# Performance work log

Hardware: AMD Instinct MI355X
Metric: run time of the kernel (lower is better)

Reference implementation:

```python
import jax, jax.numpy as jnp
import numpy as np

N_NODES = 100000
N_EDGES = 400000
IN_FEATS = 64
H_FEATS = 128
INTER = 128
NUM_CLASSES = 64


def setup_inputs() -> dict:
    key = jax.random.key(0)
    ks = jax.random.split(key, 32)
    inp = {}
    inp['gate_type'] = jax.random.randint(ks[0], (N_NODES,), 0, IN_FEATS)
    inp['src'] = jax.random.randint(ks[1], (N_EDGES,), 0, N_NODES)
    inp['dst'] = jax.random.randint(ks[2], (N_EDGES,), 0, N_NODES)
    inp['src_idx'] = jax.random.uniform(ks[3], (N_EDGES,), dtype=jnp.float32)
    inp['dst_idx'] = jax.random.uniform(ks[4], (N_EDGES,), dtype=jnp.float32)
    inp['rev'] = jax.random.uniform(ks[5], (N_EDGES,), dtype=jnp.float32)
    inp['emb'] = jax.random.normal(ks[6], (IN_FEATS, IN_FEATS), dtype=jnp.float32) * 0.05
    dims = [(IN_FEATS, H_FEATS), (H_FEATS, H_FEATS), (H_FEATS, H_FEATS), (H_FEATS, H_FEATS), (H_FEATS, NUM_CLASSES)]
    k = 7
    for i, (fi, fo) in enumerate(dims, 1):
        # xavier-normal-like scaling
        inp[f'w1_{i}'] = jax.random.normal(ks[k], (INTER, fi + 3), dtype=jnp.float32) * np.float32(np.sqrt(2.0 / (fi + 3 + INTER))); k += 1
        inp[f'w2_{i}'] = jax.random.normal(ks[k], (fo, fi + INTER), dtype=jnp.float32) * np.float32(np.sqrt(2.0 / (fi + INTER + fo))); k += 1
        inp[f'b2_{i}'] = jnp.zeros((fo,), dtype=jnp.float32); k += 1
    return inp


def _qconv(h, src, dst, w_edge, W1, W2, b2):
    # message: concat src node feats with edge feats -> [E, d+3]
    m = jnp.concatenate([h[src], w_edge], axis=1)
    # linear1 (no bias) + leaky_relu (torch default slope 0.01)
    tmp = jax.nn.leaky_relu(m @ W1.T, negative_slope=0.01)  # [E, inter]
    # mean-reduce per destination node (isolated nodes -> zeros, matching DGL)
    s = jax.ops.segment_sum(tmp, dst, num_segments=h.shape[0])
    cnt = jax.ops.segment_sum(jnp.ones((dst.shape[0],), tmp.dtype), dst, num_segments=h.shape[0])
    h_N = s / jnp.maximum(cnt, 1.0)[:, None]
    # linear2 on [h, h_N]
    return jnp.concatenate([h, h_N], axis=1) @ W2.T + b2


def reference(gate_type, src, dst, src_idx, dst_idx, rev, emb,
              w1_1, w2_1, b2_1, w1_2, w2_2, b2_2, w1_3, w2_3, b2_3,
              w1_4, w2_4, b2_4, w1_5, w2_5, b2_5):
    h = emb[gate_type]  # [N, in_feats]
    w_edge = jnp.stack([src_idx, dst_idx, rev], axis=1)  # [E, 3]
    layers = [(w1_1, w2_1, b2_1), (w1_2, w2_2, b2_2), (w1_3, w2_3, b2_3),
              (w1_4, w2_4, b2_4), (w1_5, w2_5, b2_5)]
    for i, (W1, W2, b2) in enumerate(layers):
        h = _qconv(h, src, dst, w_edge, W1, W2, b2)
        if i < 4:
            h = jax.nn.relu(h)
    return h
```

## Files before the change

kernel.cpp:

```cpp
#include <hip/hip_runtime.h>
#include <hip/hip_fp16.h>

typedef __attribute__((ext_vector_type(8))) short short8;
typedef __attribute__((ext_vector_type(4))) float f32x4;
typedef unsigned short u16;

__device__ __forceinline__ u16 f2bf(float f) {
    unsigned u = __float_as_uint(f);
    unsigned r = ((u >> 16) & 1) + 0x7FFFu;
    return (u16)((u + r) >> 16);
}

__device__ __forceinline__ void gload_lds16(const void* g, void* l) {
    __builtin_amdgcn_global_load_lds((const __attribute__((address_space(1))) unsigned int*)g,
                                     (__attribute__((address_space(3))) unsigned int*)l,
                                     16, 0, 0);
}

__device__ __forceinline__ unsigned pk_fma(unsigned a, unsigned b, unsigned c) {
    unsigned d;
    asm("v_pk_fma_f16 %0, %1, %2, %3" : "=v"(d) : "v"(a), "v"(b), "v"(c));
    return d;
}
__device__ __forceinline__ unsigned pk_mul(unsigned a, unsigned b) {
    unsigned d;
    asm("v_pk_mul_f16 %0, %1, %2" : "=v"(d) : "v"(a), "v"(b));
    return d;
}
__device__ __forceinline__ unsigned pk_max(unsigned a, unsigned b) {
    unsigned d;
    asm("v_pk_max_f16 %0, %1, %2" : "=v"(d) : "v"(a), "v"(b));
    return d;
}


__global__ void k_count(const int* __restrict__ dst, int* __restrict__ cnt, int E) {
    int i = blockIdx.x * 256 + threadIdx.x;
    if (i < E) atomicAdd(&cnt[dst[i]], 1);
}

__global__ void k_scan1(const int* __restrict__ cnt, int* __restrict__ partial, int N) {
    __shared__ int sm[256];
    int idx = blockIdx.x * 256 + threadIdx.x;
    sm[threadIdx.x] = (idx < N) ? cnt[idx] : 0;
    __syncthreads();
    for (int s = 128; s > 0; s >>= 1) {
        if (threadIdx.x < s) sm[threadIdx.x] += sm[threadIdx.x + s];
        __syncthreads();
    }
    if (threadIdx.x == 0) partial[blockIdx.x] = sm[0];
}

__global__ void k_scan2(int* __restrict__ partial, int nb) {
    __shared__ int sm[512];
    int t = threadIdx.x;
    sm[t] = (t < nb) ? partial[t] : 0;
    __syncthreads();
    for (int off = 1; off < 512; off <<= 1) {
        int v = (t >= off) ? sm[t - off] : 0;
        __syncthreads();
        sm[t] += v;
        __syncthreads();
    }
    if (t < nb) partial[t] = (t == 0) ? 0 : sm[t - 1];
}

__global__ void k_scan3(const int* __restrict__ cnt, const int* __restrict__ partial,
                        int* __restrict__ row_off, int* __restrict__ cursor,
                        float* __restrict__ invdeg, int N, int E) {
    __shared__ int sm[256];
    int idx = blockIdx.x * 256 + threadIdx.x;
    int v = (idx < N) ? cnt[idx] : 0;
    sm[threadIdx.x] = v;
    __syncthreads();
    for (int off = 1; off < 256; off <<= 1) {
        int u = (threadIdx.x >= off) ? sm[threadIdx.x - off] : 0;
        __syncthreads();
        sm[threadIdx.x] += u;
        __syncthreads();
    }
    if (idx < N) {
        int excl = partial[blockIdx.x] + sm[threadIdx.x] - v;
        row_off[idx] = excl;
        cursor[idx] = excl;
        invdeg[idx] = 1.0f / (float)((v > 1) ? v : 1);
    }
    if (idx == 0) row_off[N] = E;
}

__global__ void k_scatter(const int* __restrict__ dst, const int* __restrict__ src,
                          const float* __restrict__ sidx, const float* __restrict__ didx,
                          const float* __restrict__ rev,
                          int* __restrict__ cursor, int4* __restrict__ payload, int E) {
    int i = blockIdx.x * 256 + threadIdx.x;
    if (i < E) {
        int p = atomicAdd(&cursor[dst[i]], 1);
        unsigned hs = (unsigned)__half_as_ushort(__float2half_rn(sidx[i]));
        unsigned hd = (unsigned)__half_as_ushort(__float2half_rn(didx[i]));
        unsigned hr = (unsigned)__half_as_ushort(__float2half_rn(rev[i]));
        int4 v;
        v.x = src[i];
        v.y = (int)(hs * 0x10001u);
        v.z = (int)(hd * 0x10001u);
        v.w = (int)(hr * 0x10001u);
        payload[p] = v;
    }
}


__global__ void k_emb(const int* __restrict__ gt, const float* __restrict__ emb,
                      u16* __restrict__ h0, int N) {
    int i = blockIdx.x * 256 + threadIdx.x;
    if (i < N * 64) {
        int n = i >> 6, f = i & 63;
        h0[i] = f2bf(emb[(gt[n] << 6) | f]);
    }
}


struct WDesc {
    const float* src[10];
    u16* dst[10];
    int scols[10];
    int dcols[10];
    int n[10];
};

__global__ void k_wconv(WDesc d) {
    int seg = blockIdx.y;
    int idx = blockIdx.x * 256 + threadIdx.x;
    if (idx < d.n[seg]) {
        int dc = d.dcols[seg];
        int r = idx / dc, c = idx % dc;
        d.dst[seg][idx] = f2bf(d.src[seg][r * d.scols[seg] + c]);
    }
}

struct EDesc {
    const float* src[5];
    unsigned* dst[5];
    int ldw[5];
    int fi[5];
};

__global__ void k_wedge(EDesc d) {
    int l = blockIdx.x;
    int i = threadIdx.x;
    if (i < 192) {
        int c = i >> 6, j = i & 63;
        float a = d.src[l][(size_t)(2 * j) * d.ldw[l] + d.fi[l] + c];
        float b = d.src[l][(size_t)(2 * j + 1) * d.ldw[l] + d.fi[l] + c];
        unsigned lo = (unsigned)__half_as_ushort(__float2half_rn(a));
        unsigned hi = (unsigned)__half_as_ushort(__float2half_rn(b));
        d.dst[l][(c << 6) + j] = lo | (hi << 16);
    }
}


__global__ __launch_bounds__(256)
void k_edge(int N,
            const int* __restrict__ row_off, const int4* __restrict__ payload,
            const u16* __restrict__ g,
            const unsigned* __restrict__ W1h,
            const float* __restrict__ invdeg,
            u16* __restrict__ hN)
{
    const int t = threadIdx.x;
    const int lane = t & 63;
    const int fl = lane & 15;
    const int eg = lane >> 4;
    const int wid = blockIdx.x * (blockDim.x >> 6) + (t >> 6);
    const int nwtot = gridDim.x * (blockDim.x >> 6);
    const int per = (N + nwtot - 1) / nwtot;
    const int n0 = wid * per;
    if (n0 >= N) return;
    const int n1 = (n0 + per < N) ? (n0 + per) : N;

    const uint4 wa = *(const uint4*)&W1h[(fl << 2)];
    const uint4 wb = *(const uint4*)&W1h[64 + (fl << 2)];
    const uint4 wc = *(const uint4*)&W1h[128 + (fl << 2)];
    const unsigned c001 = ((unsigned)__half_as_ushort(__float2half_rn(0.01f))) * 0x10001u;

    int beg = row_off[n0];
    for (int n = n0; n < n1; ++n) {
        const int end = row_off[n + 1];
        float acc[8] = {0.f, 0.f, 0.f, 0.f, 0.f, 0.f, 0.f, 0.f};

        int p = beg + eg;
        int4 pl;
        if (p < end) pl = payload[p];
        while (p < end) {
            const int pn = p + 4;
            int4 plN = pl;
            if (pn < end) plN = payload[pn];
            const uint4 gv = *(const uint4*)(g + ((size_t)pl.x << 7) + (fl << 3));
            const unsigned si = (unsigned)pl.y;
            const unsigned di = (unsigned)pl.z;
            const unsigned rv = (unsigned)pl.w;
            unsigned v0 = pk_fma(wa.x, si, gv.x);
            unsigned v1 = pk_fma(wa.y, si, gv.y);
            unsigned v2 = pk_fma(wa.z, si, gv.z);
            unsigned v3 = pk_fma(wa.w, si, gv.w);
            v0 = pk_fma(wb.x, di, v0);
            v1 = pk_fma(wb.y, di, v1);
            v2 = pk_fma(wb.z, di, v2);
            v3 = pk_fma(wb.w, di, v3);
            v0 = pk_fma(wc.x, rv, v0);
            v1 = pk_fma(wc.y, rv, v1);
            v2 = pk_fma(wc.z, rv, v2);
            v3 = pk_fma(wc.w, rv, v3);
            v0 = pk_max(v0, pk_mul(v0, c001));
            v1 = pk_max(v1, pk_mul(v1, c001));
            v2 = pk_max(v2, pk_mul(v2, c001));
            v3 = pk_max(v3, pk_mul(v3, c001));
            const float2 f0 = __half22float2(*(const __half2*)&v0);
            const float2 f1 = __half22float2(*(const __half2*)&v1);
            const float2 f2 = __half22float2(*(const __half2*)&v2);
            const float2 f3 = __half22float2(*(const __half2*)&v3);
            acc[0] += f0.x; acc[1] += f0.y;
            acc[2] += f1.x; acc[3] += f1.y;
            acc[4] += f2.x; acc[5] += f2.y;
            acc[6] += f3.x; acc[7] += f3.y;
            p = pn;
            pl = plN;
        }

#pragma unroll
        for (int r = 0; r < 8; r++) {
            acc[r] += __shfl_xor(acc[r], 16, 64);
            acc[r] += __shfl_xor(acc[r], 32, 64);
        }

        if (eg == 0) {
            const float inv = invdeg[n];
            unsigned q0 = (unsigned)f2bf(acc[0] * inv) | ((unsigned)f2bf(acc[1] * inv) << 16);
            unsigned q1 = (unsigned)f2bf(acc[2] * inv) | ((unsigned)f2bf(acc[3] * inv) << 16);
            unsigned q2 = (unsigned)f2bf(acc[4] * inv) | ((unsigned)f2bf(acc[5] * inv) << 16);
            unsigned q3 = (unsigned)f2bf(acc[6] * inv) | ((unsigned)f2bf(acc[7] * inv) << 16);
            uint4 out = make_uint4(q0, q1, q2, q3);
            *(uint4*)(hN + ((size_t)n << 7) + (fl << 3)) = out;
        }
        beg = end;
    }
}


template<int K, int O, int SPLIT, int BIAS, int RELU, int OUTDT, int FUSE>
__global__ __launch_bounds__(512, 4)
void k_gemm(int M,
            const u16* __restrict__ A1, int lda1,
            const u16* __restrict__ A2, int lda2,
            const u16* __restrict__ W,
            const float* __restrict__ bias,
            void* __restrict__ Cout, int ldc,
            const u16* __restrict__ Wg,
            u16* __restrict__ Gout)
{
    constexpr int KP = K + 8;
    constexpr int HP = 136;
    constexpr int NF = O / 32;
    constexpr int WC = O / 2;
    __shared__ __align__(16) u16 Wlds[O * KP];
    __shared__ __align__(16) u16 Atile[128 * 32];

    const int t = threadIdx.x;
    const int m0 = blockIdx.x * 128;
    const int w = t >> 6, l = t & 63;
    const int wm = w & 3, wn = w >> 2;
    const int lr = l & 15, lh = l >> 4;

    for (int idx = t; idx < O * (K / 8); idx += 512) {
        int row = idx / (K / 8), ch = idx % (K / 8);
        uint4 v = *(const uint4*)(W + (size_t)row * K + ch * 8);
        *(uint4*)(&Wlds[row * KP + ch * 8]) = v;
    }

    f32x4 acc[2][NF];
#pragma unroll
    for (int mi = 0; mi < 2; mi++)
#pragma unroll
        for (int ni = 0; ni < NF; ni++) acc[mi][ni] = (f32x4){0.f, 0.f, 0.f, 0.f};

    __syncthreads();

    for (int kt = 0; kt < K / 32; ++kt) {
        const int k0 = kt * 32;
        const u16* Asrc;
        int lda, kof;
        if (k0 < SPLIT) { Asrc = A1; lda = lda1; kof = k0; }
        else            { Asrc = A2; lda = lda2; kof = k0 - SPLIT; }
        {
            int o = t * 16;
            int row = o >> 6;
            int m = m0 + row;
            m = (m < M) ? m : (M - 1);
            gload_lds16(Asrc + (size_t)m * lda + kof + ((t & 3) << 3), (void*)(Atile + (o >> 1)));
        }
        __syncthreads();

        short8 a[2], b[NF];
#pragma unroll
        for (int mi = 0; mi < 2; mi++)
            a[mi] = *(const short8*)(Atile + (wm * 32 + mi * 16 + lr) * 32 + lh * 8);
#pragma unroll
        for (int ni = 0; ni < NF; ni++)
            b[ni] = *(const short8*)(Wlds + (size_t)(wn * WC + ni * 16 + lr) * KP + k0 + lh * 8);
#pragma unroll
        for (int mi = 0; mi < 2; mi++)
#pragma unroll
            for (int ni = 0; ni < NF; ni++)
                acc[mi][ni] = __builtin_amdgcn_mfma_f32_16x16x32_bf16(a[mi], b[ni], acc[mi][ni], 0, 0, 0);
        __syncthreads();
    }

    if (FUSE) {
        for (int idx = t; idx < 128 * 16; idx += 512) {
            int row = idx >> 4, ch = idx & 15;
            uint4 v = *(const uint4*)(Wg + (size_t)row * 128 + ch * 8);
            *(uint4*)(&Wlds[row * HP + ch * 8]) = v;
        }
    }

    float bv[NF];
#pragma unroll
    for (int ni = 0; ni < NF; ni++)
        bv[ni] = BIAS ? bias[wn * WC + ni * 16 + lr] : 0.f;
#pragma unroll
    for (int mi = 0; mi < 2; mi++) {
#pragma unroll
        for (int i = 0; i < 4; i++) {
            int row = m0 + wm * 32 + mi * 16 + lh * 4 + i;
            if (row < M) {
#pragma unroll
                for (int ni = 0; ni < NF; ni++) {
                    float v = acc[mi][ni][i] + bv[ni];
                    if (RELU) v = fmaxf(v, 0.f);
                    int col = wn * WC + ni * 16 + lr;
                    if (FUSE || OUTDT == 1) ((u16*)Cout)[(size_t)row * ldc + col] = f2bf(v);
                    else if (OUTDT == 2)    ((__half*)Cout)[(size_t)row * ldc + col] = __float2half(v);
                    else                    ((float*)Cout)[(size_t)row * ldc + col] = v;
                }
            }
        }
    }

    if (FUSE) {
        __syncthreads();

        const u16* H = (const u16*)Cout;
        int hrow[2];
#pragma unroll
        for (int mi = 0; mi < 2; mi++) {
            int m = m0 + wm * 32 + mi * 16 + lr;
            hrow[mi] = (m < M) ? m : (M - 1);
        }

        f32x4 acc2[2][4];
#pragma unroll
        for (int mi = 0; mi < 2; mi++)
#pragma unroll
            for (int ni = 0; ni < 4; ni++) acc2[mi][ni] = (f32x4){0.f, 0.f, 0.f, 0.f};

#pragma unroll
        for (int kt = 0; kt < 4; ++kt) {
            const int k0 = kt * 32;
            short8 a[2], b[4];
#pragma unroll
            for (int mi = 0; mi < 2; mi++)
                a[mi] = *(const short8*)(H + (size_t)hrow[mi] * ldc + k0 + lh * 8);
#pragma unroll
            for (int ni = 0; ni < 4; ni++)
                b[ni] = *(const short8*)(Wlds + (size_t)(wn * 64 + ni * 16 + lr) * HP + k0 + lh * 8);
#pragma unroll
            for (int mi = 0; mi < 2; mi++)
#pragma unroll
                for (int ni = 0; ni < 4; ni++)
                    acc2[mi][ni] = __builtin_amdgcn_mfma_f32_16x16x32_bf16(a[mi], b[ni], acc2[mi][ni], 0, 0, 0);
        }

#pragma unroll
        for (int mi = 0; mi < 2; mi++) {
#pragma unroll
            for (int i = 0; i < 4; i++) {
                int row = m0 + wm * 32 + mi * 16 + lh * 4 + i;
                if (row < M) {
#pragma unroll
                    for (int ni = 0; ni < 4; ni++) {
                        int col = wn * 64 + ni * 16 + lr;
                        ((__half*)Gout)[(size_t)row * 128 + col] = __float2half(acc2[mi][ni][i]);
                    }
                }
            }
        }
    }
}


extern "C" void kernel_launch(void* const* d_in, const int* in_sizes, int n_in,
                              void* d_out, int out_size, void* d_ws, size_t ws_size,
                              hipStream_t stream)
{
    const int N = in_sizes[0];
    const int E = in_sizes[1];
    const int* gate = (const int*)d_in[0];
    const int* src = (const int*)d_in[1];
    const int* dst = (const int*)d_in[2];
    const float* sidx = (const float*)d_in[3];
    const float* didx = (const float*)d_in[4];
    const float* rev = (const float*)d_in[5];
    const float* emb = (const float*)d_in[6];
    const float* w1[5] = {(const float*)d_in[7], (const float*)d_in[10], (const float*)d_in[13],
                          (const float*)d_in[16], (const float*)d_in[19]};
    const float* w2[5] = {(const float*)d_in[8], (const float*)d_in[11], (const float*)d_in[14],
                          (const float*)d_in[17], (const float*)d_in[20]};
    const float* b2[5] = {(const float*)d_in[9], (const float*)d_in[12], (const float*)d_in[15],
                          (const float*)d_in[18], (const float*)d_in[21]};

    char* ws = (char*)d_ws;
    size_t off = 0;
    auto alloc = [&](size_t bytes) {
        void* p = ws + off;
        off = (off + bytes + 255) & ~(size_t)255;
        return p;
    };
    u16* hb0 = (u16*)alloc((size_t)N * 128 * 2);
    u16* hb1 = (u16*)alloc((size_t)N * 128 * 2);
    u16* hN = (u16*)alloc((size_t)N * 128 * 2);
    u16* g = (u16*)alloc((size_t)N * 128 * 2);
    int* cnt = (int*)alloc((size_t)N * 4);
    int* row_off = (int*)alloc((size_t)(N + 1) * 4);
    int* cursor = (int*)alloc((size_t)N * 4);
    int4* payload = (int4*)alloc((size_t)E * 16);
    int* partial = (int*)alloc(512 * 4);
    float* invd = (float*)alloc((size_t)N * 4);
    unsigned* w1h = (unsigned*)alloc(5 * 192 * 4);
    u16* w1b[5];
    u16* w2b[5];
    const int fis[5] = {64, 128, 128, 128, 128};
    for (int i = 0; i < 5; i++) w1b[i] = (u16*)alloc((size_t)128 * fis[i] * 2);
    for (int i = 0; i < 5; i++) {
        int fo = (i == 4) ? 64 : 128;
        w2b[i] = (u16*)alloc((size_t)fo * (fis[i] + 128) * 2);
    }

    WDesc wd;
    for (int i = 0; i < 5; i++) {
        wd.src[i] = w1[i]; wd.dst[i] = w1b[i];
        wd.scols[i] = fis[i] + 3; wd.dcols[i] = fis[i]; wd.n[i] = 128 * fis[i];
        int fo = (i == 4) ? 64 : 128;
        wd.src[5 + i] = w2[i]; wd.dst[5 + i] = w2b[i];
        wd.scols[5 + i] = fis[i] + 128; wd.dcols[5 + i] = fis[i] + 128;
        wd.n[5 + i] = fo * (fis[i] + 128);
    }
    k_wconv<<<dim3(128, 10), dim3(256), 0, stream>>>(wd);

    EDesc ed;
    for (int i = 0; i < 5; i++) {
        ed.src[i] = w1[i];
        ed.dst[i] = w1h + i * 192;
        ed.ldw[i] = fis[i] + 3;
        ed.fi[i] = fis[i];
    }
    k_wedge<<<dim3(5), dim3(192), 0, stream>>>(ed);

    hipMemsetAsync(cnt, 0, (size_t)N * 4, stream);
    k_count<<<dim3((E + 255) / 256), dim3(256), 0, stream>>>(dst, cnt, E);
    const int nb = (N + 255) / 256;
    k_scan1<<<dim3(nb), dim3(256), 0, stream>>>(cnt, partial, N);
    k_scan2<<<dim3(1), dim3(512), 0, stream>>>(partial, nb);
    k_scan3<<<dim3(nb), dim3(256), 0, stream>>>(cnt, partial, row_off, cursor, invd, N, E);
    k_scatter<<<dim3((E + 255) / 256), dim3(256), 0, stream>>>(dst, src, sidx, didx, rev, cursor, payload, E);
    k_emb<<<dim3((N * 64 + 255) / 256), dim3(256), 0, stream>>>(gate, emb, hb0, N);

    const int gg = (N + 127) / 128;
    const int eb = 2048;

    k_gemm<64, 128, 64, 0, 0, 2, 0><<<dim3(gg), dim3(512), 0, stream>>>(
        N, hb0, 64, (const u16*)nullptr, 0, w1b[0], (const float*)nullptr, g, 128,
        (const u16*)nullptr, (u16*)nullptr);
    k_edge<<<dim3(eb), dim3(256), 0, stream>>>(N, row_off, payload, g, w1h + 0 * 192, invd, hN);
    k_gemm<192, 128, 64, 1, 1, 1, 1><<<dim3(gg), dim3(512), 0, stream>>>(
        N, hb0, 64, hN, 128, w2b[0], b2[0], hb1, 128, w1b[1], g);

    u16* hcur = hb1;
    u16* hnxt = hb0;
    for (int l = 1; l < 4; ++l) {
        k_edge<<<dim3(eb), dim3(256), 0, stream>>>(N, row_off, payload, g, w1h + l * 192, invd, hN);
        k_gemm<256, 128, 128, 1, 1, 1, 1><<<dim3(gg), dim3(512), 0, stream>>>(
            N, hcur, 128, hN, 128, w2b[l], b2[l], hnxt, 128, w1b[l + 1], g);
        u16* tmp = hcur; hcur = hnxt; hnxt = tmp;
    }

    k_edge<<<dim3(eb), dim3(256), 0, stream>>>(N, row_off, payload, g, w1h + 4 * 192, invd, hN);
    k_gemm<256, 64, 128, 1, 0, 0, 0><<<dim3(gg), dim3(512), 0, stream>>>(
        N, hcur, 128, hN, 128, w2b[4], b2[4], (float*)d_out, 64,
        (const u16*)nullptr, (u16*)nullptr);
}
```

Before: 413.1 us.

## Interleave two destination nodes per wave and accumulate edge sums in packed fp16

```diff
diff --git a/kernel.cpp b/kernel.cpp
--- a/kernel.cpp
+++ b/kernel.cpp
@@ -30,6 +30,11 @@
 __device__ __forceinline__ unsigned pk_max(unsigned a, unsigned b) {
     unsigned d;
     asm("v_pk_max_f16 %0, %1, %2" : "=v"(d) : "v"(a), "v"(b));
+    return d;
+}
+__device__ __forceinline__ unsigned pk_add(unsigned a, unsigned b) {
+    unsigned d;
+    asm("v_pk_add_f16 %0, %1, %2" : "=v"(d) : "v"(a), "v"(b));
     return d;
 }
 
@@ -176,71 +181,123 @@
     if (n0 >= N) return;
     const int n1 = (n0 + per < N) ? (n0 + per) : N;
 
+    int roi = n0 + lane;
+    const int ro_l = row_off[(roi <= n1) ? roi : n1];
+
     const uint4 wa = *(const uint4*)&W1h[(fl << 2)];
     const uint4 wb = *(const uint4*)&W1h[64 + (fl << 2)];
     const uint4 wc = *(const uint4*)&W1h[128 + (fl << 2)];
     const unsigned c001 = ((unsigned)__half_as_ushort(__float2half_rn(0.01f))) * 0x10001u;
 
-    int beg = row_off[n0];
-    for (int n = n0; n < n1; ++n) {
-        const int end = row_off[n + 1];
-        float acc[8] = {0.f, 0.f, 0.f, 0.f, 0.f, 0.f, 0.f, 0.f};
-
-        int p = beg + eg;
-        int4 pl;
-        if (p < end) pl = payload[p];
-        while (p < end) {
-            const int pn = p + 4;
-            int4 plN = pl;
-            if (pn < end) plN = payload[pn];
-            const uint4 gv = *(const uint4*)(g + ((size_t)pl.x << 7) + (fl << 3));
-            const unsigned si = (unsigned)pl.y;
-            const unsigned di = (unsigned)pl.z;
-            const unsigned rv = (unsigned)pl.w;
-            unsigned v0 = pk_fma(wa.x, si, gv.x);
-            unsigned v1 = pk_fma(wa.y, si, gv.y);
-            unsigned v2 = pk_fma(wa.z, si, gv.z);
-            unsigned v3 = pk_fma(wa.w, si, gv.w);
-            v0 = pk_fma(wb.x, di, v0);
-            v1 = pk_fma(wb.y, di, v1);
-            v2 = pk_fma(wb.z, di, v2);
-            v3 = pk_fma(wb.w, di, v3);
-            v0 = pk_fma(wc.x, rv, v0);
-            v1 = pk_fma(wc.y, rv, v1);
-            v2 = pk_fma(wc.z, rv, v2);
-            v3 = pk_fma(wc.w, rv, v3);
-            v0 = pk_max(v0, pk_mul(v0, c001));
-            v1 = pk_max(v1, pk_mul(v1, c001));
-            v2 = pk_max(v2, pk_mul(v2, c001));
-            v3 = pk_max(v3, pk_mul(v3, c001));
-            const float2 f0 = __half22float2(*(const __half2*)&v0);
-            const float2 f1 = __half22float2(*(const __half2*)&v1);
-            const float2 f2 = __half22float2(*(const __half2*)&v2);
-            const float2 f3 = __half22float2(*(const __half2*)&v3);
-            acc[0] += f0.x; acc[1] += f0.y;
-            acc[2] += f1.x; acc[3] += f1.y;
-            acc[4] += f2.x; acc[5] += f2.y;
-            acc[6] += f3.x; acc[7] += f3.y;
-            p = pn;
-            pl = plN;
-        }
-
-#pragma unroll
-        for (int r = 0; r < 8; r++) {
-            acc[r] += __shfl_xor(acc[r], 16, 64);
-            acc[r] += __shfl_xor(acc[r], 32, 64);
-        }
-
+    int na, pa, ea, qa;
+    int4 pla;
+    uint4 gva;
+    unsigned accA[4] = {0u, 0u, 0u, 0u};
+    int nb_, pb, eb, qb;
+    int4 plb;
+    uint4 gvb;
+    unsigned accB[4] = {0u, 0u, 0u, 0u};
+
+    auto prime = [&](int n, int& p, int& e, int& q, int4& pl, uint4& gv) {
+        const int idx = n - n0;
+        const int b = __shfl(ro_l, idx, 64);
+        e = __shfl(ro_l, idx + 1, 64);
+        p = b + eg;
+        q = (e - b + 3) >> 2;
+        if (p < e) {
+            pl = payload[p];
+            gv = *(const uint4*)(g + ((size_t)pl.x << 7) + (fl << 3));
+        }
+    };
+
+    auto quadf = [&](const int4& pl, const uint4& gv, unsigned* acc) {
+        const unsigned si = (unsigned)pl.y;
+        const unsigned di = (unsigned)pl.z;
+        const unsigned rv = (unsigned)pl.w;
+        unsigned v0 = pk_fma(wa.x, si, gv.x);
+        unsigned v1 = pk_fma(wa.y, si, gv.y);
+        unsigned v2 = pk_fma(wa.z, si, gv.z);
+        unsigned v3 = pk_fma(wa.w, si, gv.w);
+        v0 = pk_fma(wb.x, di, v0);
+        v1 = pk_fma(wb.y, di, v1);
+        v2 = pk_fma(wb.z, di, v2);
+        v3 = pk_fma(wb.w, di, v3);
+        v0 = pk_fma(wc.x, rv, v0);
+        v1 = pk_fma(wc.y, rv, v1);
+        v2 = pk_fma(wc.z, rv, v2);
+        v3 = pk_fma(wc.w, rv, v3);
+        v0 = pk_max(v0, pk_mul(v0, c001));
+        v1 = pk_max(v1, pk_mul(v1, c001));
+        v2 = pk_max(v2, pk_mul(v2, c001));
+        v3 = pk_max(v3, pk_mul(v3, c001));
+        acc[0] = pk_add(acc[0], v0);
+        acc[1] = pk_add(acc[1], v1);
+        acc[2] = pk_add(acc[2], v2);
+        acc[3] = pk_add(acc[3], v3);
+    };
+
+    auto finishf = [&](int n, unsigned* acc) {
+#pragma unroll
+        for (int r = 0; r < 4; r++) {
+            acc[r] = pk_add(acc[r], (unsigned)__shfl_xor((int)acc[r], 16, 64));
+            acc[r] = pk_add(acc[r], (unsigned)__shfl_xor((int)acc[r], 32, 64));
+        }
         if (eg == 0) {
             const float inv = invdeg[n];
-            unsigned q0 = (unsigned)f2bf(acc[0] * inv) | ((unsigned)f2bf(acc[1] * inv) << 16);
-            unsigned q1 = (unsigned)f2bf(acc[2] * inv) | ((unsigned)f2bf(acc[3] * inv) << 16);
-            unsigned q2 = (unsigned)f2bf(acc[4] * inv) | ((unsigned)f2bf(acc[5] * inv) << 16);
-            unsigned q3 = (unsigned)f2bf(acc[6] * inv) | ((unsigned)f2bf(acc[7] * inv) << 16);
+            const float2 f0 = __half22float2(*(const __half2*)&acc[0]);
+            const float2 f1 = __half22float2(*(const __half2*)&acc[1]);
+            const float2 f2 = __half22float2(*(const __half2*)&acc[2]);
+            const float2 f3 = __half22float2(*(const __half2*)&acc[3]);
+            unsigned q0 = (unsigned)f2bf(f0.x * inv) | ((unsigned)f2bf(f0.y * inv) << 16);
+            unsigned q1 = (unsigned)f2bf(f1.x * inv) | ((unsigned)f2bf(f1.y * inv) << 16);
+            unsigned q2 = (unsigned)f2bf(f2.x * inv) | ((unsigned)f2bf(f2.y * inv) << 16);
+            unsigned q3 = (unsigned)f2bf(f3.x * inv) | ((unsigned)f2bf(f3.y * inv) << 16);
             uint4 out = make_uint4(q0, q1, q2, q3);
             *(uint4*)(hN + ((size_t)n << 7) + (fl << 3)) = out;
         }
-        beg = end;
+        acc[0] = acc[1] = acc[2] = acc[3] = 0u;
+    };
+
+    na = n0;
+    prime(na, pa, ea, qa, pla, gva);
+    nb_ = n0 + 1;
+    bool doneB = (nb_ >= n1);
+    if (!doneB) prime(nb_, pb, eb, qb, plb, gvb);
+    bool doneA = false;
+
+    while (!doneA || !doneB) {
+        if (!doneA) {
+            if (qa > 0) {
+                if (pa < ea) quadf(pla, gva, accA);
+                pa += 4;
+                qa--;
+                if (qa > 0 && pa < ea) {
+                    pla = payload[pa];
+                    gva = *(const uint4*)(g + ((size_t)pla.x << 7) + (fl << 3));
+                }
+            } else {
+                finishf(na, accA);
+                na += 2;
+                if (na < n1) prime(na, pa, ea, qa, pla, gva);
+                else doneA = true;
+            }
+        }
+        if (!doneB) {
+            if (qb > 0) {
+                if (pb < eb) quadf(plb, gvb, accB);
+                pb += 4;
+                qb--;
+                if (qb > 0 && pb < eb) {
+                    plb = payload[pb];
+                    gvb = *(const uint4*)(g + ((size_t)plb.x << 7) + (fl << 3));
+                }
+            } else {
+                finishf(nb_, accB);
+                nb_ += 2;
+                if (nb_ < n1) prime(nb_, pb, eb, qb, plb, gvb);
+                else doneB = true;
+            }
+        }
     }
 }
 
```

Result: slower. 451.3 us (+9.2%).

## Precompute per-gate-type layer-1 projection table and drop first GEMM

Applied to the files above, without the earlier changes.

```diff
diff --git a/kernel.cpp b/kernel.cpp
--- a/kernel.cpp
+++ b/kernel.cpp
@@ -108,12 +108,29 @@
 }
 
 
-__global__ void k_emb(const int* __restrict__ gt, const float* __restrict__ emb,
-                      u16* __restrict__ h0, int N) {
+__global__ void k_tab(const float* __restrict__ emb, const float* __restrict__ w1,
+                      u16* __restrict__ T0, u16* __restrict__ T1) {
+    int t = threadIdx.x;
+    for (int i = t; i < 64 * 64; i += 256) T0[i] = f2bf(emb[i]);
+    for (int i = t; i < 64 * 128; i += 256) {
+        int ty = i >> 7, j = i & 127;
+        float acc = 0.f;
+#pragma unroll 8
+        for (int k = 0; k < 64; k++)
+            acc = fmaf(emb[ty * 64 + k], w1[j * 67 + k], acc);
+        T1[i] = (u16)__half_as_ushort(__float2half_rn(acc));
+    }
+}
+
+__global__ void k_emb2(const int* __restrict__ gt, const uint4* __restrict__ T0,
+                       const uint4* __restrict__ T1, uint4* __restrict__ h0,
+                       uint4* __restrict__ g, int N) {
     int i = blockIdx.x * 256 + threadIdx.x;
-    if (i < N * 64) {
-        int n = i >> 6, f = i & 63;
-        h0[i] = f2bf(emb[(gt[n] << 6) | f]);
+    if (i < N * 16) {
+        int n = i >> 4, c = i & 15;
+        int ty = gt[n];
+        g[i] = T1[ty * 16 + c];
+        if (c < 8) h0[n * 8 + c] = T0[ty * 8 + c];
     }
 }
 
@@ -434,6 +451,8 @@
     int* partial = (int*)alloc(512 * 4);
     float* invd = (float*)alloc((size_t)N * 4);
     unsigned* w1h = (unsigned*)alloc(5 * 192 * 4);
+    u16* T0 = (u16*)alloc(64 * 64 * 2);
+    u16* T1 = (u16*)alloc(64 * 128 * 2);
     u16* w1b[5];
     u16* w2b[5];
     const int fis[5] = {64, 128, 128, 128, 128};
@@ -462,6 +481,7 @@
         ed.fi[i] = fis[i];
     }
     k_wedge<<<dim3(5), dim3(192), 0, stream>>>(ed);
+    k_tab<<<dim3(1), dim3(256), 0, stream>>>(emb, w1[0], T0, T1);
 
     hipMemsetAsync(cnt, 0, (size_t)N * 4, stream);
     k_count<<<dim3((E + 255) / 256), dim3(256), 0, stream>>>(dst, cnt, E);
@@ -470,14 +490,12 @@
     k_scan2<<<dim3(1), dim3(512), 0, stream>>>(partial, nb);
     k_scan3<<<dim3(nb), dim3(256), 0, stream>>>(cnt, partial, row_off, cursor, invd, N, E);
     k_scatter<<<dim3((E + 255) / 256), dim3(256), 0, stream>>>(dst, src, sidx, didx, rev, cursor, payload, E);
-    k_emb<<<dim3((N * 64 + 255) / 256), dim3(256), 0, stream>>>(gate, emb, hb0, N);
+    k_emb2<<<dim3((N * 16 + 255) / 256), dim3(256), 0, stream>>>(
+        gate, (const uint4*)T0, (const uint4*)T1, (uint4*)hb0, (uint4*)g, N);
 
     const int gg = (N + 127) / 128;
     const int eb = 2048;
 
-    k_gemm<64, 128, 64, 0, 0, 2, 0><<<dim3(gg), dim3(512), 0, stream>>>(
-        N, hb0, 64, (const u16*)nullptr, 0, w1b[0], (const float*)nullptr, g, 128,
-        (const u16*)nullptr, (u16*)nullptr);
     k_edge<<<dim3(eb), dim3(256), 0, stream>>>(N, row_off, payload, g, w1h + 0 * 192, invd, hN);
     k_gemm<192, 128, 64, 1, 1, 1, 1><<<dim3(gg), dim3(512), 0, stream>>>(
         N, hb0, 64, hN, 128, w2b[0], b2[0], hb1, 128, w1b[1], g);
```

After: 446.3 us. 8.0% more time.
